# Performance work log

Measured on AMD Instinct MI355X. Metric: run time of the kernel, lower is better.

Reference implementation:

```python
import jax, jax.numpy as jnp
import numpy as np

N = 10000       # nodes
E = 640000      # edges (before self-loops)
D_IN = 128
H1 = 128
H2 = 64
EMB = 64
NEG_SLOPE = 0.2  # PyG GATConv default


def setup_inputs() -> dict:
    key = jax.random.key(0)
    ks = jax.random.split(key, 12)
    s = 0.05
    return {
        "x": jax.random.normal(ks[0], (N, D_IN), dtype=jnp.float32),
        "edge_index": jax.random.randint(ks[1], (2, E), 0, N, dtype=jnp.int64),
        "W1": jax.random.normal(ks[2], (D_IN, H1), dtype=jnp.float32) * s,
        "a_src1": jax.random.normal(ks[3], (H1,), dtype=jnp.float32) * s,
        "a_dst1": jax.random.normal(ks[4], (H1,), dtype=jnp.float32) * s,
        "b1": jnp.zeros((H1,), dtype=jnp.float32),
        "W2": jax.random.normal(ks[5], (H1, H2), dtype=jnp.float32) * s,
        "a_src2": jax.random.normal(ks[6], (H2,), dtype=jnp.float32) * s,
        "a_dst2": jax.random.normal(ks[7], (H2,), dtype=jnp.float32) * s,
        "b2": jnp.zeros((H2,), dtype=jnp.float32),
        "Wp": jax.random.normal(ks[8], (H2, EMB), dtype=jnp.float32) * s,
        "bp": jnp.zeros((EMB,), dtype=jnp.float32),
    }


def _gat_conv(x, src, dst, W, a_src, a_dst, b):
    # x: [N, Din] -> h: [N, Dout]
    h = x @ W
    # edge-wise attention logits (PyG: alpha_src from source j, alpha_dst from target i)
    logits = jax.nn.leaky_relu((h @ a_src)[src] + (h @ a_dst)[dst], NEG_SLOPE)  # [E+N]
    # softmax over incoming edges of each destination node (numerically stable)
    m = jax.ops.segment_max(logits, dst, num_segments=N)
    e = jnp.exp(logits - m[dst])
    z = jax.ops.segment_sum(e, dst, num_segments=N)
    w = e / z[dst]                                                              # [E+N]
    # weighted scatter-add of source features into destinations
    out = jax.ops.segment_sum(w[:, None] * h[src], dst, num_segments=N)         # [N, Dout]
    return out + b


def reference(x, edge_index, W1, a_src1, a_dst1, b1, W2, a_src2, a_dst2, b2, Wp, bp):
    # add self-loops (PyG GATConv default add_self_loops=True)
    loop = jnp.arange(N, dtype=edge_index.dtype)
    ei = jnp.concatenate([edge_index, jnp.stack([loop, loop])], axis=1)
    src, dst = ei[0], ei[1]
    x1 = jax.nn.relu(_gat_conv(x, src, dst, W1, a_src1, a_dst1, b1))
    x2 = jax.nn.relu(_gat_conv(x1, src, dst, W2, a_src2, a_dst2, b2))
    return x2 @ Wp + bp  # [N, EMB]
```

## Files before the change

kernel.cpp:

```cpp
#include <hip/hip_runtime.h>
#include <hip/hip_bf16.h>

#define NNODES 10000
#define NEDGES 640000
#define NTOT   (NNODES + NEDGES)
#define D_IN 128
#define H1 128
#define H2 64
#define EMB 64

#define NBUCKET 160
#define BCAP    8192
#define CHUNK   4096


__global__ __launch_bounds__(256) void bucket_kernel(const int* __restrict__ ei,
                                                     int* __restrict__ bucket_cursor,
                                                     int* __restrict__ bucket_arr) {
    __shared__ int ordered[CHUNK];
    __shared__ int hist[NBUCKET];
    __shared__ int binStart[NBUCKET];
    __shared__ int bincur[NBUCKET];
    __shared__ int gcur[NBUCKET];
    __shared__ int wtmp[4];

    int tid = threadIdx.x;
    int base = blockIdx.x * CHUNK;
    int n = NTOT - base; if (n > CHUNK) n = CHUNK;

    int rec[CHUNK / 256];
#pragma unroll
    for (int k = 0; k < CHUNK / 256; ++k) {
        int i = base + k * 256 + tid;
        int r = 0;
        if (i < NTOT) {
            int s, d;
            if (i < NEDGES) { s = ei[i]; d = ei[NEDGES + i]; }
            else            { s = d = i - NEDGES; }
            r = (d << 16) | s;
        }
        rec[k] = r;
    }

    for (int b = tid; b < NBUCKET; b += 256) hist[b] = 0;
    __syncthreads();
#pragma unroll
    for (int k = 0; k < CHUNK / 256; ++k) {
        int i = base + k * 256 + tid;
        if (i < NTOT) atomicAdd(&hist[rec[k] >> 22], 1);
    }
    __syncthreads();

    {
        int v = (tid < NBUCKET) ? hist[tid] : 0;
        int lane = tid & 63, w = tid >> 6;
        int inc = v;
        for (int o = 1; o < 64; o <<= 1) {
            int t = __shfl_up(inc, o, 64);
            if (lane >= o) inc += t;
        }
        if (lane == 63) wtmp[w] = inc;
        __syncthreads();
        int pre = 0;
        for (int i = 0; i < w; ++i) pre += wtmp[i];
        if (tid < NBUCKET) {
            binStart[tid] = pre + inc - v;
            bincur[tid]   = pre + inc - v;
        }
    }
    __syncthreads();

#pragma unroll
    for (int k = 0; k < CHUNK / 256; ++k) {
        int i = base + k * 256 + tid;
        if (i < NTOT) {
            int pos = atomicAdd(&bincur[rec[k] >> 22], 1);
            ordered[pos] = rec[k];
        }
    }
    __syncthreads();

    for (int b = tid; b < NBUCKET; b += 256) {
        int c = hist[b];
        gcur[b] = c ? atomicAdd(&bucket_cursor[b], c) : 0;
    }
    __syncthreads();

#pragma unroll
    for (int k = 0; k < CHUNK / 256; ++k) {
        int i = k * 256 + tid;
        if (i < n) {
            int r = ordered[i];
            int b = r >> 22;
            bucket_arr[b * BCAP + gcur[b] + (i - binStart[b])] = r;
        }
    }
}


__global__ __launch_bounds__(256) void build_kernel(const int* __restrict__ bucket_cursor,
                                                    const int* __restrict__ bucket_arr,
                                                    int* __restrict__ rowptr,
                                                    int* __restrict__ csr_src) {
    __shared__ int sbase[NBUCKET];
    __shared__ int wtmp[4];
    __shared__ int hist[64];
    __shared__ int bincur[64];
    int tid = threadIdx.x;
    int b = blockIdx.x;

    {
        int v = (tid < NBUCKET) ? bucket_cursor[tid] : 0;
        int lane = tid & 63, w = tid >> 6;
        int inc = v;
        for (int o = 1; o < 64; o <<= 1) {
            int t = __shfl_up(inc, o, 64);
            if (lane >= o) inc += t;
        }
        if (lane == 63) wtmp[w] = inc;
        __syncthreads();
        int pre = 0;
        for (int i = 0; i < w; ++i) pre += wtmp[i];
        if (tid < NBUCKET) sbase[tid] = pre + inc - v;
    }
    __syncthreads();

    int cnt = bucket_cursor[b];
    int base = sbase[b];
    const int* arr = bucket_arr + b * BCAP;

    if (tid < 64) hist[tid] = 0;
    __syncthreads();
    for (int i = tid; i < cnt; i += 256) atomicAdd(&hist[(arr[i] >> 16) & 63], 1);
    __syncthreads();

    if (tid < 64) {
        int v = hist[tid];
        int inc = v;
        for (int o = 1; o < 64; o <<= 1) {
            int t = __shfl_up(inc, o, 64);
            if (tid >= o) inc += t;
        }
        bincur[tid] = inc - v;
        int node = b * 64 + tid;
        if (node < NNODES) rowptr[node] = base + inc - v;
    }
    if (b == 0 && tid == 0) rowptr[NNODES] = NTOT;
    __syncthreads();

    for (int i = tid; i < cnt; i += 256) {
        int r = arr[i];
        int pos = base + atomicAdd(&bincur[(r >> 16) & 63], 1);
        csr_src[pos] = r & 0xFFFF;
    }
}


template <int K, int NC, bool BIAS, bool DOTS>
__global__ __launch_bounds__(256) void gemm_kernel(const float* __restrict__ A,
                                                   const float* __restrict__ B,
                                                   const float* __restrict__ bias,
                                                   float* __restrict__ C, int M,
                                                   const float* __restrict__ a_src,
                                                   const float* __restrict__ a_dst,
                                                   float* __restrict__ as,
                                                   float* __restrict__ ad) {
    __shared__ float Alds[32 * K];
    __shared__ float Blds[K * NC];
    int tid = threadIdx.x;
    int row0 = blockIdx.x * 32;

    const float4* A4 = (const float4*)(A + (size_t)row0 * K);
    float4* Al4 = (float4*)Alds;
    constexpr int A4N = 32 * K / 4;
    for (int idx = tid; idx < A4N; idx += 256) {
        int r = idx / (K / 4);
        float4 z4 = {0.f, 0.f, 0.f, 0.f};
        Al4[idx] = (row0 + r < M) ? A4[idx] : z4;
    }
    const float4* B4 = (const float4*)B;
    float4* Bl4 = (float4*)Blds;
    constexpr int B4N = K * NC / 4;
    for (int idx = tid; idx < B4N; idx += 256) Bl4[idx] = B4[idx];
    __syncthreads();

    int tx = tid & 31;
    int ty = tid >> 5;
    constexpr int CPT = NC / 32;
    float acc[4][CPT];
#pragma unroll
    for (int rr = 0; rr < 4; ++rr)
#pragma unroll
        for (int cc = 0; cc < CPT; ++cc) acc[rr][cc] = 0.f;

    for (int k = 0; k < K; ++k) {
        float bv[CPT];
        const float* Bk = &Blds[k * NC + tx * CPT];
#pragma unroll
        for (int cc = 0; cc < CPT; ++cc) bv[cc] = Bk[cc];
#pragma unroll
        for (int rr = 0; rr < 4; ++rr) {
            float a = Alds[(ty + 8 * rr) * K + k];
#pragma unroll
            for (int cc = 0; cc < CPT; ++cc) acc[rr][cc] = fmaf(a, bv[cc], acc[rr][cc]);
        }
    }

#pragma unroll
    for (int rr = 0; rr < 4; ++rr) {
        int gr = row0 + ty + 8 * rr;
        if (gr < M) {
#pragma unroll
            for (int cc = 0; cc < CPT; ++cc) {
                int c = tx * CPT + cc;
                float v = acc[rr][cc];
                if (BIAS) v += bias[c];
                C[(size_t)gr * NC + c] = v;
            }
        }
    }

    if (DOTS) {
        float asv[CPT], adv[CPT];
#pragma unroll
        for (int cc = 0; cc < CPT; ++cc) {
            asv[cc] = a_src[tx * CPT + cc];
            adv[cc] = a_dst[tx * CPT + cc];
        }
#pragma unroll
        for (int rr = 0; rr < 4; ++rr) {
            float s1 = 0.f, s2 = 0.f;
#pragma unroll
            for (int cc = 0; cc < CPT; ++cc) {
                s1 = fmaf(acc[rr][cc], asv[cc], s1);
                s2 = fmaf(acc[rr][cc], adv[cc], s2);
            }
#pragma unroll
            for (int o = 1; o < 32; o <<= 1) {
                s1 += __shfl_xor(s1, o, 64);
                s2 += __shfl_xor(s2, o, 64);
            }
            int gr = row0 + ty + 8 * rr;
            if (tx == 0 && gr < M) { as[gr] = s1; ad[gr] = s2; }
        }
    }
}


template <int H>
__global__ __launch_bounds__(256) void agg_kernel(const int* __restrict__ rowptr,
                                                  const int* __restrict__ csr_src,
                                                  const float* __restrict__ h,
                                                  const float* __restrict__ as,
                                                  const float* __restrict__ ad,
                                                  const float* __restrict__ bias,
                                                  float* __restrict__ out) {
    int wid = (blockIdx.x * blockDim.x + threadIdx.x) >> 6;
    int lane = threadIdx.x & 63;
    if (wid >= NNODES) return;
    int beg = rowptr[wid];
    int end = rowptr[wid + 1];
    float ad_d = ad[wid];

    const float2* h2 = (const float2*)h;
    float z = 0.f, acc0 = 0.f, acc1 = 0.f;

    for (int chunk = beg; chunk < end; chunk += 64) {
        int myj = chunk + lane;
        int cnt = end - chunk; if (cnt > 64) cnt = 64;
        int s_l = 0;
        float e_l = 0.f;
        if (myj < end) {
            s_l = csr_src[myj];
            float l = as[s_l] + ad_d;
            l = (l > 0.f) ? l : 0.2f * l;
            e_l = __expf(l);
        }
        z += e_l;
        int cnt8 = (cnt + 7) & ~7;
        for (int t = 0; t < cnt8; t += 8) {
#pragma unroll
            for (int u = 0; u < 8; ++u) {
                int tt = __builtin_amdgcn_readfirstlane(t + u);
                int s = __builtin_amdgcn_readlane(s_l, tt);
                float e = __int_as_float(
                    __builtin_amdgcn_readlane(__float_as_int(e_l), tt));
                if (H == 128) {
                    float2 v = h2[(size_t)s * 64 + lane];
                    acc0 = fmaf(e, v.x, acc0);
                    acc1 = fmaf(e, v.y, acc1);
                } else {
                    float v = h[(size_t)s * H + lane];
                    acc0 = fmaf(e, v, acc0);
                }
            }
        }
    }
    for (int o = 32; o; o >>= 1) z += __shfl_xor(z, o, 64);
    float rz = 1.f / z;
    if (H == 128) {
        float2 bb = ((const float2*)bias)[lane];
        float2 o2;
        o2.x = fmaxf(acc0 * rz + bb.x, 0.f);
        o2.y = fmaxf(acc1 * rz + bb.y, 0.f);
        ((float2*)out)[(size_t)wid * 64 + lane] = o2;
    } else {
        float o0 = fmaxf(acc0 * rz + bias[lane], 0.f);
        out[(size_t)wid * H + lane] = o0;
    }
}


extern "C" void kernel_launch(void* const* d_in, const int* in_sizes, int n_in,
                              void* d_out, int out_size, void* d_ws, size_t ws_size,
                              hipStream_t stream) {
    const float* x      = (const float*)d_in[0];
    const int*   ei     = (const int*)d_in[1];
    const float* W1     = (const float*)d_in[2];
    const float* a_src1 = (const float*)d_in[3];
    const float* a_dst1 = (const float*)d_in[4];
    const float* b1     = (const float*)d_in[5];
    const float* W2     = (const float*)d_in[6];
    const float* a_src2 = (const float*)d_in[7];
    const float* a_dst2 = (const float*)d_in[8];
    const float* b2     = (const float*)d_in[9];
    const float* Wp     = (const float*)d_in[10];
    const float* bp     = (const float*)d_in[11];
    float* out = (float*)d_out;

    char* ws = (char*)d_ws;
    size_t off = 0;
    auto alloc = [&](size_t bytes) {
        void* p = ws + off;
        off = (off + bytes + 255) & ~(size_t)255;
        return p;
    };
    int*   bucket_cursor = (int*)alloc(NBUCKET * 4);
    int*   bucket_arr    = (int*)alloc((size_t)NBUCKET * BCAP * 4);
    int*   rowptr  = (int*)alloc((NNODES + 1) * 4);
    int*   csr_src = (int*)alloc((size_t)NTOT * 4);
    float* h1      = (float*)alloc((size_t)NNODES * H1 * 4);
    float* as1     = (float*)alloc(NNODES * 4);
    float* ad1     = (float*)alloc(NNODES * 4);
    float* x1      = (float*)alloc((size_t)NNODES * H1 * 4);
    float* h2      = (float*)alloc((size_t)NNODES * H2 * 4);
    float* as2     = (float*)alloc(NNODES * 4);
    float* ad2     = (float*)alloc(NNODES * 4);
    float* x2      = (float*)alloc((size_t)NNODES * H2 * 4);
    (void)ws_size;

    const int TB = 256;
    int gemm_b = (NNODES + 31) / 32;
    int wave_b = (NNODES * 64 + TB - 1) / TB;
    int p1_b = (NTOT + CHUNK - 1) / CHUNK;

    hipMemsetAsync(bucket_cursor, 0, NBUCKET * 4, stream);
    bucket_kernel<<<p1_b, TB, 0, stream>>>(ei, bucket_cursor, bucket_arr);
    build_kernel<<<(NNODES + 63) / 64, TB, 0, stream>>>(bucket_cursor,
                                                        bucket_arr, rowptr, csr_src);

    gemm_kernel<D_IN, H1, false, true><<<gemm_b, TB, 0, stream>>>(
        x, W1, nullptr, h1, NNODES, a_src1, a_dst1, as1, ad1);
    agg_kernel<H1><<<wave_b, TB, 0, stream>>>(rowptr, csr_src, h1, as1, ad1, b1, x1);

    gemm_kernel<H1, H2, false, true><<<gemm_b, TB, 0, stream>>>(
        x1, W2, nullptr, h2, NNODES, a_src2, a_dst2, as2, ad2);
    agg_kernel<H2><<<wave_b, TB, 0, stream>>>(rowptr, csr_src, h2, as2, ad2, b2, x2);

    gemm_kernel<H2, EMB, true, false><<<gemm_b, TB, 0, stream>>>(
        x2, Wp, bp, out, NNODES, nullptr, nullptr, nullptr, nullptr);
}
```

Baseline: 182.9 us.

## Fuse GEMMs into aggregation kernels, merge bucketing with GEMM1, store features in fp16

Bucketing of edges and the first GEMM now run as disjoint block ranges of a single launch that shares LDS through a union. The layer-2 GEMM is fused into the layer-1 aggregation epilogue, and the final projection into the layer-2 aggregation epilogue, using per-wave rows against weights staged in LDS. Intermediate features h1 and h2 are stored as fp16 to halve the gather traffic in aggregation. This removes three launches and the x1/x2 round trips through memory. In exchange every aggregation block reloads the full weight matrix into LDS, and fp16 rounding adds error.

```diff
diff --git a/kernel.cpp b/kernel.cpp
--- a/kernel.cpp
+++ b/kernel.cpp
@@ -12,20 +12,23 @@
 #define NBUCKET 160
 #define BCAP    8192
 #define CHUNK   4096
-
-
-__global__ __launch_bounds__(256) void bucket_kernel(const int* __restrict__ ei,
-                                                     int* __restrict__ bucket_cursor,
-                                                     int* __restrict__ bucket_arr) {
-    __shared__ int ordered[CHUNK];
-    __shared__ int hist[NBUCKET];
-    __shared__ int binStart[NBUCKET];
-    __shared__ int bincur[NBUCKET];
-    __shared__ int gcur[NBUCKET];
-    __shared__ int wtmp[4];
-
+#define NCHUNK  ((NTOT + CHUNK - 1) / CHUNK)
+#define NTILE   ((NNODES + 31) / 32)
+
+typedef _Float16 half2v __attribute__((ext_vector_type(2)));
+typedef _Float16 half4v __attribute__((ext_vector_type(4)));
+
+union SMemA {
+    struct { int ordered[CHUNK]; int hist[NBUCKET]; int binStart[NBUCKET];
+             int bincur[NBUCKET]; int gcur[NBUCKET]; int wtmp[4]; } p1;
+    struct { float A[32 * 64]; float B[64 * 128]; } g;
+};
+
+__device__ __forceinline__ void bucket_chunk(SMemA& sm, int c, const int* __restrict__ ei,
+                                             int* __restrict__ bucket_cursor,
+                                             int* __restrict__ bucket_arr) {
     int tid = threadIdx.x;
-    int base = blockIdx.x * CHUNK;
+    int base = c * CHUNK;
     int n = NTOT - base; if (n > CHUNK) n = CHUNK;
 
     int rec[CHUNK / 256];
@@ -42,30 +45,30 @@
         rec[k] = r;
     }
 
-    for (int b = tid; b < NBUCKET; b += 256) hist[b] = 0;
+    for (int b = tid; b < NBUCKET; b += 256) sm.p1.hist[b] = 0;
     __syncthreads();
 #pragma unroll
     for (int k = 0; k < CHUNK / 256; ++k) {
         int i = base + k * 256 + tid;
-        if (i < NTOT) atomicAdd(&hist[rec[k] >> 22], 1);
+        if (i < NTOT) atomicAdd(&sm.p1.hist[rec[k] >> 22], 1);
     }
     __syncthreads();
 
     {
-        int v = (tid < NBUCKET) ? hist[tid] : 0;
+        int v = (tid < NBUCKET) ? sm.p1.hist[tid] : 0;
         int lane = tid & 63, w = tid >> 6;
         int inc = v;
         for (int o = 1; o < 64; o <<= 1) {
             int t = __shfl_up(inc, o, 64);
             if (lane >= o) inc += t;
         }
-        if (lane == 63) wtmp[w] = inc;
+        if (lane == 63) sm.p1.wtmp[w] = inc;
         __syncthreads();
         int pre = 0;
-        for (int i = 0; i < w; ++i) pre += wtmp[i];
+        for (int i = 0; i < w; ++i) pre += sm.p1.wtmp[i];
         if (tid < NBUCKET) {
-            binStart[tid] = pre + inc - v;
-            bincur[tid]   = pre + inc - v;
+            sm.p1.binStart[tid] = pre + inc - v;
+            sm.p1.bincur[tid]   = pre + inc - v;
         }
     }
     __syncthreads();
@@ -74,15 +77,15 @@
     for (int k = 0; k < CHUNK / 256; ++k) {
         int i = base + k * 256 + tid;
         if (i < NTOT) {
-            int pos = atomicAdd(&bincur[rec[k] >> 22], 1);
-            ordered[pos] = rec[k];
+            int pos = atomicAdd(&sm.p1.bincur[rec[k] >> 22], 1);
+            sm.p1.ordered[pos] = rec[k];
         }
     }
     __syncthreads();
 
     for (int b = tid; b < NBUCKET; b += 256) {
-        int c = hist[b];
-        gcur[b] = c ? atomicAdd(&bucket_cursor[b], c) : 0;
+        int cc = sm.p1.hist[b];
+        sm.p1.gcur[b] = cc ? atomicAdd(&bucket_cursor[b], cc) : 0;
     }
     __syncthreads();
 
@@ -90,13 +93,111 @@
     for (int k = 0; k < CHUNK / 256; ++k) {
         int i = k * 256 + tid;
         if (i < n) {
-            int r = ordered[i];
+            int r = sm.p1.ordered[i];
             int b = r >> 22;
-            bucket_arr[b * BCAP + gcur[b] + (i - binStart[b])] = r;
-        }
-    }
-}
-
+            bucket_arr[b * BCAP + sm.p1.gcur[b] + (i - sm.p1.binStart[b])] = r;
+        }
+    }
+}
+
+__device__ __forceinline__ void gemm1_tile(SMemA& sm, int t,
+                                           const float* __restrict__ x,
+                                           const float* __restrict__ W1,
+                                           const float* __restrict__ a_src1,
+                                           const float* __restrict__ a_dst1,
+                                           _Float16* __restrict__ h1h,
+                                           float* __restrict__ as1,
+                                           float* __restrict__ ad1) {
+    int tid = threadIdx.x;
+    int row0 = t * 32;
+    int tx = tid & 31;
+    int ty = tid >> 5;
+    float acc[4][4];
+#pragma unroll
+    for (int rr = 0; rr < 4; ++rr)
+#pragma unroll
+        for (int cc = 0; cc < 4; ++cc) acc[rr][cc] = 0.f;
+
+    for (int kk = 0; kk < D_IN; kk += 64) {
+        float4* Al4 = (float4*)sm.g.A;
+        for (int idx = tid; idx < 32 * 16; idx += 256) {
+            int r = idx >> 4, c = idx & 15;
+            float4 z4 = {0.f, 0.f, 0.f, 0.f};
+            Al4[idx] = (row0 + r < NNODES)
+                ? ((const float4*)(x + (size_t)(row0 + r) * D_IN + kk))[c] : z4;
+        }
+        float4* Bl4 = (float4*)sm.g.B;
+        const float4* B4 = (const float4*)(W1 + (size_t)kk * H1);
+        for (int idx = tid; idx < 64 * H1 / 4; idx += 256) Bl4[idx] = B4[idx];
+        __syncthreads();
+
+        for (int k = 0; k < 64; ++k) {
+            float bv[4];
+            const float* Bk = &sm.g.B[k * H1 + tx * 4];
+#pragma unroll
+            for (int cc = 0; cc < 4; ++cc) bv[cc] = Bk[cc];
+#pragma unroll
+            for (int rr = 0; rr < 4; ++rr) {
+                float a = sm.g.A[(ty + 8 * rr) * 64 + k];
+#pragma unroll
+                for (int cc = 0; cc < 4; ++cc) acc[rr][cc] = fmaf(a, bv[cc], acc[rr][cc]);
+            }
+        }
+        __syncthreads();
+    }
+
+#pragma unroll
+    for (int rr = 0; rr < 4; ++rr) {
+        int gr = row0 + ty + 8 * rr;
+        if (gr < NNODES) {
+            half4v hv;
+            hv.x = (_Float16)acc[rr][0]; hv.y = (_Float16)acc[rr][1];
+            hv.z = (_Float16)acc[rr][2]; hv.w = (_Float16)acc[rr][3];
+            ((half4v*)(h1h + (size_t)gr * H1))[tx] = hv;
+        }
+    }
+
+    float asv[4], adv[4];
+#pragma unroll
+    for (int cc = 0; cc < 4; ++cc) {
+        asv[cc] = a_src1[tx * 4 + cc];
+        adv[cc] = a_dst1[tx * 4 + cc];
+    }
+#pragma unroll
+    for (int rr = 0; rr < 4; ++rr) {
+        float s1 = 0.f, s2 = 0.f;
+#pragma unroll
+        for (int cc = 0; cc < 4; ++cc) {
+            s1 = fmaf(acc[rr][cc], asv[cc], s1);
+            s2 = fmaf(acc[rr][cc], adv[cc], s2);
+        }
+#pragma unroll
+        for (int o = 1; o < 32; o <<= 1) {
+            s1 += __shfl_xor(s1, o, 64);
+            s2 += __shfl_xor(s2, o, 64);
+        }
+        int gr = row0 + ty + 8 * rr;
+        if (tx == 0 && gr < NNODES) { as1[gr] = s1; ad1[gr] = s2; }
+    }
+}
+
+__global__ __launch_bounds__(256) void csr_gemm1_kernel(const int* __restrict__ ei,
+                                                        int* __restrict__ bucket_cursor,
+                                                        int* __restrict__ bucket_arr,
+                                                        const float* __restrict__ x,
+                                                        const float* __restrict__ W1,
+                                                        const float* __restrict__ a_src1,
+                                                        const float* __restrict__ a_dst1,
+                                                        _Float16* __restrict__ h1h,
+                                                        float* __restrict__ as1,
+                                                        float* __restrict__ ad1) {
+    __shared__ SMemA sm;
+    int bid = blockIdx.x;
+    if (bid < NCHUNK)
+        bucket_chunk(sm, bid, ei, bucket_cursor, bucket_arr);
+    else
+        gemm1_tile(sm, bid - NCHUNK, x, W1, a_src1, a_dst1, h1h, as1, ad1);
+}
 
 __global__ __launch_bounds__(256) void build_kernel(const int* __restrict__ bucket_cursor,
                                                     const int* __restrict__ bucket_arr,
@@ -155,124 +256,40 @@
     }
 }
 
-
-template <int K, int NC, bool BIAS, bool DOTS>
-__global__ __launch_bounds__(256) void gemm_kernel(const float* __restrict__ A,
-                                                   const float* __restrict__ B,
-                                                   const float* __restrict__ bias,
-                                                   float* __restrict__ C, int M,
-                                                   const float* __restrict__ a_src,
-                                                   const float* __restrict__ a_dst,
-                                                   float* __restrict__ as,
-                                                   float* __restrict__ ad) {
-    __shared__ float Alds[32 * K];
-    __shared__ float Blds[K * NC];
+__global__ __launch_bounds__(256) void agg1_gemm2_kernel(const int* __restrict__ rowptr,
+                                                         const int* __restrict__ csr_src,
+                                                         const _Float16* __restrict__ h1h,
+                                                         const float* __restrict__ as1,
+                                                         const float* __restrict__ ad1,
+                                                         const float* __restrict__ b1,
+                                                         const float* __restrict__ W2,
+                                                         const float* __restrict__ a_src2,
+                                                         const float* __restrict__ a_dst2,
+                                                         _Float16* __restrict__ h2h,
+                                                         float* __restrict__ as2,
+                                                         float* __restrict__ ad2) {
+    __shared__ float Wlds[H1 * H2];
+    __shared__ float xrow[4][H1];
     int tid = threadIdx.x;
-    int row0 = blockIdx.x * 32;
-
-    const float4* A4 = (const float4*)(A + (size_t)row0 * K);
-    float4* Al4 = (float4*)Alds;
-    constexpr int A4N = 32 * K / 4;
-    for (int idx = tid; idx < A4N; idx += 256) {
-        int r = idx / (K / 4);
-        float4 z4 = {0.f, 0.f, 0.f, 0.f};
-        Al4[idx] = (row0 + r < M) ? A4[idx] : z4;
-    }
-    const float4* B4 = (const float4*)B;
-    float4* Bl4 = (float4*)Blds;
-    constexpr int B4N = K * NC / 4;
-    for (int idx = tid; idx < B4N; idx += 256) Bl4[idx] = B4[idx];
-    __syncthreads();
-
-    int tx = tid & 31;
-    int ty = tid >> 5;
-    constexpr int CPT = NC / 32;
-    float acc[4][CPT];
-#pragma unroll
-    for (int rr = 0; rr < 4; ++rr)
-#pragma unroll
-        for (int cc = 0; cc < CPT; ++cc) acc[rr][cc] = 0.f;
-
-    for (int k = 0; k < K; ++k) {
-        float bv[CPT];
-        const float* Bk = &Blds[k * NC + tx * CPT];
-#pragma unroll
-        for (int cc = 0; cc < CPT; ++cc) bv[cc] = Bk[cc];
-#pragma unroll
-        for (int rr = 0; rr < 4; ++rr) {
-            float a = Alds[(ty + 8 * rr) * K + k];
-#pragma unroll
-            for (int cc = 0; cc < CPT; ++cc) acc[rr][cc] = fmaf(a, bv[cc], acc[rr][cc]);
-        }
-    }
-
-#pragma unroll
-    for (int rr = 0; rr < 4; ++rr) {
-        int gr = row0 + ty + 8 * rr;
-        if (gr < M) {
-#pragma unroll
-            for (int cc = 0; cc < CPT; ++cc) {
-                int c = tx * CPT + cc;
-                float v = acc[rr][cc];
-                if (BIAS) v += bias[c];
-                C[(size_t)gr * NC + c] = v;
-            }
-        }
-    }
-
-    if (DOTS) {
-        float asv[CPT], adv[CPT];
-#pragma unroll
-        for (int cc = 0; cc < CPT; ++cc) {
-            asv[cc] = a_src[tx * CPT + cc];
-            adv[cc] = a_dst[tx * CPT + cc];
-        }
-#pragma unroll
-        for (int rr = 0; rr < 4; ++rr) {
-            float s1 = 0.f, s2 = 0.f;
-#pragma unroll
-            for (int cc = 0; cc < CPT; ++cc) {
-                s1 = fmaf(acc[rr][cc], asv[cc], s1);
-                s2 = fmaf(acc[rr][cc], adv[cc], s2);
-            }
-#pragma unroll
-            for (int o = 1; o < 32; o <<= 1) {
-                s1 += __shfl_xor(s1, o, 64);
-                s2 += __shfl_xor(s2, o, 64);
-            }
-            int gr = row0 + ty + 8 * rr;
-            if (tx == 0 && gr < M) { as[gr] = s1; ad[gr] = s2; }
-        }
-    }
-}
-
-
-template <int H>
-__global__ __launch_bounds__(256) void agg_kernel(const int* __restrict__ rowptr,
-                                                  const int* __restrict__ csr_src,
-                                                  const float* __restrict__ h,
-                                                  const float* __restrict__ as,
-                                                  const float* __restrict__ ad,
-                                                  const float* __restrict__ bias,
-                                                  float* __restrict__ out) {
-    int wid = (blockIdx.x * blockDim.x + threadIdx.x) >> 6;
-    int lane = threadIdx.x & 63;
-    if (wid >= NNODES) return;
-    int beg = rowptr[wid];
-    int end = rowptr[wid + 1];
-    float ad_d = ad[wid];
-
-    const float2* h2 = (const float2*)h;
+    {
+        const float4* W4 = (const float4*)W2;
+        float4* Wl4 = (float4*)Wlds;
+        for (int idx = tid; idx < H1 * H2 / 4; idx += 256) Wl4[idx] = W4[idx];
+    }
+    int wv = tid >> 6, lane = tid & 63;
+    int wid = blockIdx.x * 4 + wv;
+    int beg = rowptr[wid], end = rowptr[wid + 1];
+    float ad_d = ad1[wid];
     float z = 0.f, acc0 = 0.f, acc1 = 0.f;
+    const half2v* h1p = (const half2v*)h1h;
 
     for (int chunk = beg; chunk < end; chunk += 64) {
         int myj = chunk + lane;
         int cnt = end - chunk; if (cnt > 64) cnt = 64;
-        int s_l = 0;
-        float e_l = 0.f;
+        int s_l = 0; float e_l = 0.f;
         if (myj < end) {
             s_l = csr_src[myj];
-            float l = as[s_l] + ad_d;
+            float l = as1[s_l] + ad_d;
             l = (l > 0.f) ? l : 0.2f * l;
             e_l = __expf(l);
         }
@@ -285,29 +302,100 @@
                 int s = __builtin_amdgcn_readlane(s_l, tt);
                 float e = __int_as_float(
                     __builtin_amdgcn_readlane(__float_as_int(e_l), tt));
-                if (H == 128) {
-                    float2 v = h2[(size_t)s * 64 + lane];
-                    acc0 = fmaf(e, v.x, acc0);
-                    acc1 = fmaf(e, v.y, acc1);
-                } else {
-                    float v = h[(size_t)s * H + lane];
-                    acc0 = fmaf(e, v, acc0);
-                }
+                half2v hp = h1p[(size_t)s * 64 + lane];
+                acc0 = fmaf(e, (float)hp.x, acc0);
+                acc1 = fmaf(e, (float)hp.y, acc1);
             }
         }
     }
     for (int o = 32; o; o >>= 1) z += __shfl_xor(z, o, 64);
     float rz = 1.f / z;
-    if (H == 128) {
-        float2 bb = ((const float2*)bias)[lane];
-        float2 o2;
-        o2.x = fmaxf(acc0 * rz + bb.x, 0.f);
-        o2.y = fmaxf(acc1 * rz + bb.y, 0.f);
-        ((float2*)out)[(size_t)wid * 64 + lane] = o2;
-    } else {
-        float o0 = fmaxf(acc0 * rz + bias[lane], 0.f);
-        out[(size_t)wid * H + lane] = o0;
-    }
+    float2 bb = ((const float2*)b1)[lane];
+    float v0 = fmaxf(acc0 * rz + bb.x, 0.f);
+    float v1 = fmaxf(acc1 * rz + bb.y, 0.f);
+    ((float2*)xrow[wv])[lane] = make_float2(v0, v1);
+    __syncthreads();
+
+    float hacc = 0.f;
+    const float* xr = xrow[wv];
+    for (int k = 0; k < H1; k += 4) {
+        float4 xq = *(const float4*)&xr[k];
+        hacc = fmaf(xq.x, Wlds[(k + 0) * H2 + lane], hacc);
+        hacc = fmaf(xq.y, Wlds[(k + 1) * H2 + lane], hacc);
+        hacc = fmaf(xq.z, Wlds[(k + 2) * H2 + lane], hacc);
+        hacc = fmaf(xq.w, Wlds[(k + 3) * H2 + lane], hacc);
+    }
+    float s1 = hacc * a_src2[lane];
+    float s2 = hacc * a_dst2[lane];
+    for (int o = 32; o; o >>= 1) {
+        s1 += __shfl_xor(s1, o, 64);
+        s2 += __shfl_xor(s2, o, 64);
+    }
+    if (lane == 0) { as2[wid] = s1; ad2[wid] = s2; }
+    h2h[(size_t)wid * H2 + lane] = (_Float16)hacc;
+}
+
+__global__ __launch_bounds__(256) void agg2_proj_kernel(const int* __restrict__ rowptr,
+                                                        const int* __restrict__ csr_src,
+                                                        const _Float16* __restrict__ h2h,
+                                                        const float* __restrict__ as2,
+                                                        const float* __restrict__ ad2,
+                                                        const float* __restrict__ b2,
+                                                        const float* __restrict__ Wp,
+                                                        const float* __restrict__ bp,
+                                                        float* __restrict__ out) {
+    __shared__ float Wlds[H2 * EMB];
+    __shared__ float xrow[4][H2];
+    int tid = threadIdx.x;
+    {
+        const float4* W4 = (const float4*)Wp;
+        float4* Wl4 = (float4*)Wlds;
+        for (int idx = tid; idx < H2 * EMB / 4; idx += 256) Wl4[idx] = W4[idx];
+    }
+    int wv = tid >> 6, lane = tid & 63;
+    int wid = blockIdx.x * 4 + wv;
+    int beg = rowptr[wid], end = rowptr[wid + 1];
+    float ad_d = ad2[wid];
+    float z = 0.f, acc = 0.f;
+
+    for (int chunk = beg; chunk < end; chunk += 64) {
+        int myj = chunk + lane;
+        int cnt = end - chunk; if (cnt > 64) cnt = 64;
+        int s_l = 0; float e_l = 0.f;
+        if (myj < end) {
+            s_l = csr_src[myj];
+            float l = as2[s_l] + ad_d;
+            l = (l > 0.f) ? l : 0.2f * l;
+            e_l = __expf(l);
+        }
+        z += e_l;
+        int cnt8 = (cnt + 7) & ~7;
+        for (int t = 0; t < cnt8; t += 8) {
+#pragma unroll
+            for (int u = 0; u < 8; ++u) {
+                int tt = __builtin_amdgcn_readfirstlane(t + u);
+                int s = __builtin_amdgcn_readlane(s_l, tt);
+                float e = __int_as_float(
+                    __builtin_amdgcn_readlane(__float_as_int(e_l), tt));
+                acc = fmaf(e, (float)h2h[(size_t)s * H2 + lane], acc);
+            }
+        }
+    }
+    for (int o = 32; o; o >>= 1) z += __shfl_xor(z, o, 64);
+    float x2v = fmaxf(acc * (1.f / z) + b2[lane], 0.f);
+    xrow[wv][lane] = x2v;
+    __syncthreads();
+
+    float oacc = 0.f;
+    const float* xr = xrow[wv];
+    for (int k = 0; k < H2; k += 4) {
+        float4 xq = *(const float4*)&xr[k];
+        oacc = fmaf(xq.x, Wlds[(k + 0) * EMB + lane], oacc);
+        oacc = fmaf(xq.y, Wlds[(k + 1) * EMB + lane], oacc);
+        oacc = fmaf(xq.z, Wlds[(k + 2) * EMB + lane], oacc);
+        oacc = fmaf(xq.w, Wlds[(k + 3) * EMB + lane], oacc);
+    }
+    out[(size_t)wid * EMB + lane] = oacc + bp[lane];
 }
 
 
@@ -335,38 +423,33 @@
         off = (off + bytes + 255) & ~(size_t)255;
         return p;
     };
-    int*   bucket_cursor = (int*)alloc(NBUCKET * 4);
-    int*   bucket_arr    = (int*)alloc((size_t)NBUCKET * BCAP * 4);
-    int*   rowptr  = (int*)alloc((NNODES + 1) * 4);
-    int*   csr_src = (int*)alloc((size_t)NTOT * 4);
-    float* h1      = (float*)alloc((size_t)NNODES * H1 * 4);
-    float* as1     = (float*)alloc(NNODES * 4);
-    float* ad1     = (float*)alloc(NNODES * 4);
-    float* x1      = (float*)alloc((size_t)NNODES * H1 * 4);
-    float* h2      = (float*)alloc((size_t)NNODES * H2 * 4);
-    float* as2     = (float*)alloc(NNODES * 4);
-    float* ad2     = (float*)alloc(NNODES * 4);
-    float* x2      = (float*)alloc((size_t)NNODES * H2 * 4);
+    int*      bucket_cursor = (int*)alloc(NBUCKET * 4);
+    int*      bucket_arr    = (int*)alloc((size_t)NBUCKET * BCAP * 4);
+    int*      rowptr  = (int*)alloc((NNODES + 1) * 4);
+    int*      csr_src = (int*)alloc((size_t)NTOT * 4);
+    _Float16* h1h     = (_Float16*)alloc((size_t)NNODES * H1 * 2);
+    float*    as1     = (float*)alloc(NNODES * 4);
+    float*    ad1     = (float*)alloc(NNODES * 4);
+    _Float16* h2h     = (_Float16*)alloc((size_t)NNODES * H2 * 2);
+    float*    as2     = (float*)alloc(NNODES * 4);
+    float*    ad2     = (float*)alloc(NNODES * 4);
     (void)ws_size;
 
     const int TB = 256;
-    int gemm_b = (NNODES + 31) / 32;
-    int wave_b = (NNODES * 64 + TB - 1) / TB;
-    int p1_b = (NTOT + CHUNK - 1) / CHUNK;
+    int wave_b = NNODES / 4;
 
     hipMemsetAsync(bucket_cursor, 0, NBUCKET * 4, stream);
-    bucket_kernel<<<p1_b, TB, 0, stream>>>(ei, bucket_cursor, bucket_arr);
+
+    csr_gemm1_kernel<<<NCHUNK + NTILE, TB, 0, stream>>>(
+        ei, bucket_cursor, bucket_arr, x, W1, a_src1, a_dst1, h1h, as1, ad1);
+
     build_kernel<<<(NNODES + 63) / 64, TB, 0, stream>>>(bucket_cursor,
                                                         bucket_arr, rowptr, csr_src);
 
-    gemm_kernel<D_IN, H1, false, true><<<gemm_b, TB, 0, stream>>>(
-        x, W1, nullptr, h1, NNODES, a_src1, a_dst1, as1, ad1);
-    agg_kernel<H1><<<wave_b, TB, 0, stream>>>(rowptr, csr_src, h1, as1, ad1, b1, x1);
-
-    gemm_kernel<H1, H2, false, true><<<gemm_b, TB, 0, stream>>>(
-        x1, W2, nullptr, h2, NNODES, a_src2, a_dst2, as2, ad2);
-    agg_kernel<H2><<<wave_b, TB, 0, stream>>>(rowptr, csr_src, h2, as2, ad2, b2, x2);
-
-    gemm_kernel<H2, EMB, true, false><<<gemm_b, TB, 0, stream>>>(
-        x2, Wp, bp, out, NNODES, nullptr, nullptr, nullptr, nullptr);
-}
+    agg1_gemm2_kernel<<<wave_b, TB, 0, stream>>>(rowptr, csr_src, h1h, as1, ad1,
+                                                 b1, W2, a_src2, a_dst2,
+                                                 h2h, as2, ad2);
+
+    agg2_proj_kernel<<<wave_b, TB, 0, stream>>>(rowptr, csr_src, h2h, as2, ad2,
+                                                b2, Wp, bp, out);
+}
```

Result: faster. 162.9 us (-10.9%).
